# Optimization experiments

Measured on AMD Instinct MI355X. Metric: run time of the kernel, lower is better.

The kernel has to match this reference:

```python
import jax, jax.numpy as jnp
import numpy as np

SEQ, BATCH, HIDDEN = 2048, 1, 4096
NUM_HEADS, NUM_KV_HEADS, HEAD_DIM = 32, 8, 128
Q_PER_GROUP = NUM_HEADS // NUM_KV_HEADS  # 4
TOTAL_PROJ = NUM_KV_HEADS * (Q_PER_GROUP + 2) * HEAD_DIM  # 6144


def setup_inputs() -> dict:
    key = jax.random.key(0)
    k1, k2, k3 = jax.random.split(key, 3)
    tokens = jax.random.normal(k1, (SEQ, BATCH, HIDDEN), dtype=jnp.float32)
    # xavier-ish scaling so activations stay sane
    weight_qkv = jax.random.normal(k2, (TOTAL_PROJ, HIDDEN), dtype=jnp.float32) * (2.0 / (TOTAL_PROJ + HIDDEN)) ** 0.5
    weight_proj = jax.random.normal(k3, (HIDDEN, NUM_HEADS * HEAD_DIM), dtype=jnp.float32) * (2.0 / (HIDDEN + NUM_HEADS * HEAD_DIM)) ** 0.5
    return {"tokens": tokens, "weight_qkv": weight_qkv, "weight_proj": weight_proj}


def reference(tokens, weight_qkv, weight_proj):
    S, B, H = tokens.shape
    scale = 1.0 / HEAD_DIM ** 0.5
    # QKV projection with interleaved GQA layout: per KV group [q0..q_{g-1}, k, v]
    qkv = jnp.einsum('sbh,ph->sbp', tokens, weight_qkv)
    qkv = qkv.reshape(S, B, NUM_KV_HEADS, Q_PER_GROUP + 2, HEAD_DIM)
    q = qkv[:, :, :, :Q_PER_GROUP, :].reshape(S, B, NUM_HEADS, HEAD_DIM)
    k = qkv[:, :, :, Q_PER_GROUP, :]       # [S,B,KVH,D]
    v = qkv[:, :, :, Q_PER_GROUP + 1, :]
    # repeat_interleave KV heads to match Q heads (GQA)
    k = jnp.repeat(k, Q_PER_GROUP, axis=2)
    v = jnp.repeat(v, Q_PER_GROUP, axis=2)
    # [S,B,H,D] -> [B,H,S,D]
    q = q.transpose(1, 2, 0, 3)
    k = k.transpose(1, 2, 0, 3)
    v = v.transpose(1, 2, 0, 3)
    scores = jnp.einsum('bhsd,bhtd->bhst', q, k) * scale
    causal = jnp.tril(jnp.ones((S, S), dtype=bool))
    scores = jnp.where(causal, scores, jnp.finfo(scores.dtype).min)
    attn = jax.nn.softmax(scores, axis=-1)
    out = jnp.einsum('bhst,bhtd->bhsd', attn, v)
    # [B,H,S,D] -> [S,B,H*D]
    out = out.transpose(2, 0, 1, 3).reshape(S, B, NUM_HEADS * HEAD_DIM)
    return jnp.einsum('sbe,he->sbh', out, weight_proj)
```

## Files before the change

### kernel.cpp

```cpp
#include <hip/hip_runtime.h>
#include <hip/hip_bf16.h>
#include <stdint.h>

#define SEQ 2048
#define HIDDEN 4096
#define NHEADS 32
#define HD 128
#define QKV_LD 6144
#define OUT_LD 4096

typedef __attribute__((ext_vector_type(8))) short short8;
typedef __attribute__((ext_vector_type(4))) short short4v;
typedef __attribute__((ext_vector_type(4))) float f32x4;
typedef __attribute__((ext_vector_type(4))) int int4v;
typedef __attribute__((ext_vector_type(2))) unsigned int uint2v;
typedef __attribute__((ext_vector_type(4))) float float4v;

__device__ __forceinline__ short f2bf(float f) {
  uint32_t u = __builtin_bit_cast(uint32_t, f);
  u += 0x7fff + ((u >> 16) & 1);
  return (short)(u >> 16);
}

__global__ void cast_kernel(const float* __restrict__ in, short* __restrict__ out, int n4) {
  int stride = gridDim.x * blockDim.x;
  for (int i = blockIdx.x * blockDim.x + threadIdx.x; i < n4; i += stride) {
    float4v v = ((const float4v*)in)[i];
    short4v o;
    o[0] = f2bf(v[0]); o[1] = f2bf(v[1]); o[2] = f2bf(v[2]); o[3] = f2bf(v[3]);
    ((short4v*)out)[i] = o;
  }
}

template <typename OT, int NBF>
__global__ __launch_bounds__(512, 2) void gemm256b(const short* __restrict__ A,
                                                   const short* __restrict__ B,
                                                   OT* __restrict__ C,
                                                   int M, int N, int K, int NT) {
  __shared__ __align__(16) short lds[32768 + NBF * 8192];
  const int tid = threadIdx.x;
  const int w = tid >> 6, lane = tid & 63;
  const int wr = w >> 2, wc = w & 3;
  const int llo = lane & 15, lhi = lane >> 4;

  const int nwg = gridDim.x;
  const int cpx = nwg >> 3;
  const int work = ((int)blockIdx.x & 7) * cpx + ((int)blockIdx.x >> 3);
  const int mt = work / NT, nt = work % NT;
  const size_t arow0 = (size_t)mt * 256, brow0 = (size_t)nt * (NBF * 64);
  const short* Ab = A + arow0 * K;
  const short* Bb = B + brow0 * K;

  f32x4 acc[8][NBF] = {};

  auto STAGE_A = [&](int kt, int j) {
    const int bufd = kt & 1;
    const int r0 = (j << 6) + (w << 3);
    const int row = r0 + (lane >> 3);
    const short* src = Ab + (size_t)row * K + (kt << 6) + (((lane & 7) ^ (row & 7)) << 3);
    short* dst = lds + (bufd << 14) + r0 * 64;
    __builtin_amdgcn_global_load_lds(
        (const __attribute__((address_space(1))) uint32_t*)src,
        (__attribute__((address_space(3))) uint32_t*)dst, 16, 0, 0);
  };
  auto STAGE_B = [&](int kt, int j) {
    const int bufd = kt & 1;
    const int r0 = (j << 6) + (w << 3);
    const int row = r0 + (lane >> 3);
    const short* src = Bb + (size_t)row * K + (kt << 6) + (((lane & 7) ^ (row & 7)) << 3);
    short* dst = lds + 32768 + bufd * (NBF << 12) + r0 * 64;
    __builtin_amdgcn_global_load_lds(
        (const __attribute__((address_space(1))) uint32_t*)src,
        (__attribute__((address_space(3))) uint32_t*)dst, 16, 0, 0);
  };
  auto STAGE = [&](int kt) {
#pragma unroll
    for (int j = 0; j < 4; j++) STAGE_A(kt, j);
#pragma unroll
    for (int j = 0; j < NBF; j++) STAGE_B(kt, j);
  };

  auto LDA = [&](int bufd, int m, int kk) -> short8 {
    const int row = (wr << 7) + (m << 4) + llo;
    const int ch = ((kk << 2) + lhi) ^ (row & 7);
    return *(const short8*)(lds + (bufd << 14) + row * 64 + (ch << 3));
  };
  auto LDB = [&](int bufd, int n, int kk) -> short8 {
    const int row = wc * (NBF << 4) + (n << 4) + llo;
    const int ch = ((kk << 2) + lhi) ^ (row & 7);
    return *(const short8*)(lds + 32768 + bufd * (NBF << 12) + row * 64 + (ch << 3));
  };

  STAGE(0);
  STAGE(1);
  if constexpr (NBF == 3) asm volatile("s_waitcnt vmcnt(7)" ::: "memory");
  else                    asm volatile("s_waitcnt vmcnt(6)" ::: "memory");
  __builtin_amdgcn_s_barrier();

  const int NKT = K >> 6;
  for (int kt = 0; kt < NKT; ++kt) {
    const int bufd = kt & 1;
    short8 b_[NBF][2];
#pragma unroll
    for (int n = 0; n < NBF; n++) { b_[n][0] = LDB(bufd, n, 0); b_[n][1] = LDB(bufd, n, 1); }
#pragma unroll
    for (int m = 0; m < 8; m++) {
      short8 a0 = LDA(bufd, m, 0);
      short8 a1 = LDA(bufd, m, 1);
#pragma unroll
      for (int n = 0; n < NBF; n++) {
        acc[m][n] = __builtin_amdgcn_mfma_f32_16x16x32_bf16(a0, b_[n][0], acc[m][n], 0, 0, 0);
        acc[m][n] = __builtin_amdgcn_mfma_f32_16x16x32_bf16(a1, b_[n][1], acc[m][n], 0, 0, 0);
      }
    }
    asm volatile("s_waitcnt lgkmcnt(0)" ::: "memory");
    __builtin_amdgcn_s_barrier();
    if (kt + 2 < NKT) STAGE(kt + 2);
    if (kt + 1 < NKT) {
      if (kt + 2 < NKT) {
        if constexpr (NBF == 3) asm volatile("s_waitcnt vmcnt(7)" ::: "memory");
        else                    asm volatile("s_waitcnt vmcnt(6)" ::: "memory");
      } else {
        asm volatile("s_waitcnt vmcnt(0)" ::: "memory");
      }
      __builtin_amdgcn_s_barrier();
    }
  }

#pragma unroll
  for (int m = 0; m < 8; m++)
#pragma unroll
    for (int n = 0; n < NBF; n++)
#pragma unroll
      for (int r = 0; r < 4; r++) {
        const size_t row = arow0 + (wr << 7) + (m << 4) + (lhi << 2) + r;
        const size_t col = brow0 + wc * (NBF << 4) + (n << 4) + llo;
        const float v = acc[m][n][r];
        if constexpr (sizeof(OT) == 2) C[row * N + col] = f2bf(v);
        else                           C[row * N + col] = v;
      }
}

__global__ __launch_bounds__(512) void attn_fwd(const short* __restrict__ qkv,
                                                short* __restrict__ aout) {
  const int qt = gridDim.y - 1 - blockIdx.y;
  const int h = blockIdx.x;
  const int kvh = h >> 2, g = h & 3;
  const int tid = threadIdx.x;
  const int wave = tid >> 6, lane = tid & 63;
  const int lhi = lane >> 4, llo = lane & 15;

  __shared__ __align__(16) short Ksm[2][64 * 128];
  __shared__ __align__(16) short Vsm[2][64 * 128];
  __shared__ __align__(16) short Psm[8][16 * 72];

  const float scale = 0.08838834764831845f;

  const int qrow = qt * 128 + wave * 16 + llo;
  const short* qbase = qkv + (size_t)qrow * QKV_LD + (kvh * 6 + g) * HD;
  short8 qf[4];
#pragma unroll
  for (int kk = 0; kk < 4; kk++) qf[kk] = *(const short8*)(qbase + kk * 32 + lhi * 8);

  f32x4 o[8] = {};
  float mrow[4], lrow[4];
#pragma unroll
  for (int r = 0; r < 4; r++) { mrow[r] = -1e30f; lrow[r] = 0.f; }

  const short* Kg = qkv + (kvh * 6 + 4) * HD;
  const short* Vg = qkv + (kvh * 6 + 5) * HD;

  auto STAGE_K = [&](int t, int buf) {
#pragma unroll
    for (int c = 0; c < 2; c++) {
      const int call = wave * 2 + c;
      const int row = call * 4 + lhi;
      const int sc = llo ^ (row & 7);
      __builtin_amdgcn_global_load_lds(
          (const __attribute__((address_space(1))) uint32_t*)(Kg + (size_t)(t * 64 + row) * QKV_LD + sc * 8),
          (__attribute__((address_space(3))) uint32_t*)(&Ksm[buf][0] + call * 512), 16, 0, 0);
    }
  };
  short8 vreg[2];
  auto LOAD_V = [&](int t) {
#pragma unroll
    for (int c = 0; c < 2; c++) {
      const int idx = c * 512 + tid;
      const int vr = idx >> 4;
      vreg[c] = *(const short8*)(Vg + (size_t)(t * 64 + vr) * QKV_LD + (idx & 15) * 8);
    }
  };
  auto WRITE_V = [&](int buf) {
#pragma unroll
    for (int c = 0; c < 2; c++) {
      const int idx = c * 512 + tid;
      const int vr = idx >> 4, vc = idx & 15;
      *(short8*)(&Vsm[buf][0] + ((vr >> 2) * 8 + (vc >> 1)) * 64 + (vr & 3) * 16 + (vc & 1) * 8) = vreg[c];
    }
  };

  const uint32_t vlane0 = (uint32_t)(uintptr_t)(__attribute__((address_space(3))) short*)(&Vsm[0][0])
                          + (uint32_t)(lhi * 2048 + llo * 8);

  STAGE_K(0, 0);
  LOAD_V(0);
  asm volatile("s_waitcnt vmcnt(0)" ::: "memory");
  WRITE_V(0);
  __syncthreads();

  const int ntiles = 2 * qt + 2;
  const int qpos0 = qt * 128 + wave * 16 + lhi * 4;
  for (int t = 0; t < ntiles; t++) {
    const int cur = t & 1, nxt = cur ^ 1;
    const bool pf = (t + 1 < ntiles);
    if (pf) { STAGE_K(t + 1, nxt); LOAD_V(t + 1); }

    const short* Kc = &Ksm[cur][0];
    f32x4 s[4] = {};
#pragma unroll
    for (int n = 0; n < 4; n++) {
#pragma unroll
      for (int kk = 0; kk < 4; kk++) {
        const int krow = n * 16 + llo;
        const int ch = (kk * 4 + lhi) ^ (krow & 7);
        short8 kf = *(const short8*)(Kc + krow * 128 + ch * 8);
        s[n] = __builtin_amdgcn_mfma_f32_16x16x32_bf16(qf[kk], kf, s[n], 0, 0, 0);
      }
    }

    float sv[4][4];
    const bool diag = (t >= 2 * qt);
#pragma unroll
    for (int n = 0; n < 4; n++)
#pragma unroll
      for (int r = 0; r < 4; r++) {
        float x = s[n][r] * scale;
        if (diag && (t * 64 + n * 16 + llo > qpos0 + r)) x = -1e30f;
        sv[n][r] = x;
      }

    float rm4[4];
#pragma unroll
    for (int r = 0; r < 4; r++) {
      float rm = fmaxf(fmaxf(sv[0][r], sv[1][r]), fmaxf(sv[2][r], sv[3][r]));
#pragma unroll
      for (int msk = 1; msk < 16; msk <<= 1) rm = fmaxf(rm, __shfl_xor(rm, msk));
      rm4[r] = rm;
    }
    bool need = false;
#pragma unroll
    for (int r = 0; r < 4; r++) need = need || (rm4[r] > mrow[r] + 8.0f);
    if (__any(need)) {
#pragma unroll
      for (int r = 0; r < 4; r++) {
        const float mnew = fmaxf(mrow[r], rm4[r]);
        const float a = __expf(mrow[r] - mnew);
        mrow[r] = mnew;
        lrow[r] *= a;
#pragma unroll
        for (int nn = 0; nn < 8; nn++) o[nn][r] *= a;
      }
    }
#pragma unroll
    for (int r = 0; r < 4; r++) {
      float rs = 0.f;
#pragma unroll
      for (int n = 0; n < 4; n++) {
        float p = __expf(sv[n][r] - mrow[r]);
        sv[n][r] = p;
        rs += p;
      }
#pragma unroll
      for (int msk = 1; msk < 16; msk <<= 1) rs += __shfl_xor(rs, msk);
      lrow[r] += rs;
    }

    short* P = &Psm[wave][0];
#pragma unroll
    for (int n = 0; n < 4; n++)
#pragma unroll
      for (int r = 0; r < 4; r++)
        P[(lhi * 4 + r) * 72 + n * 16 + llo] = f2bf(sv[n][r]);

    short8 pa0 = *(const short8*)(P + llo * 72 + lhi * 8);
    short8 pa1 = *(const short8*)(P + llo * 72 + 32 + lhi * 8);
    const uint32_t vlane = vlane0 + (uint32_t)(cur * 16384);
#pragma unroll
    for (int ks = 0; ks < 2; ks++) {
      uint2v vr_[8][2];
#pragma unroll
      for (int nn = 0; nn < 8; nn++)
#pragma unroll
        for (int hh = 0; hh < 2; hh++) {
          uint32_t a = vlane + (uint32_t)(ks * 8192 + hh * 1024 + nn * 128);
          asm volatile("ds_read_b64_tr_b16 %0, %1" : "=v"(vr_[nn][hh]) : "v"(a));
        }
      asm volatile("s_waitcnt lgkmcnt(0)" ::: "memory");
      __builtin_amdgcn_sched_barrier(0);
      const short8 pa = ks ? pa1 : pa0;
#pragma unroll
      for (int nn = 0; nn < 8; nn++) {
        int4v tv;
        tv[0] = (int)vr_[nn][0][0]; tv[1] = (int)vr_[nn][0][1];
        tv[2] = (int)vr_[nn][1][0]; tv[3] = (int)vr_[nn][1][1];
        o[nn] = __builtin_amdgcn_mfma_f32_16x16x32_bf16(pa, __builtin_bit_cast(short8, tv), o[nn], 0, 0, 0);
      }
    }

    if (pf) {
      asm volatile("s_waitcnt vmcnt(0)" ::: "memory");
      __syncthreads();
      WRITE_V(nxt);
      __syncthreads();
    }
  }

#pragma unroll
  for (int nn = 0; nn < 8; nn++)
#pragma unroll
    for (int r = 0; r < 4; r++) {
      const size_t row = qt * 128 + wave * 16 + lhi * 4 + r;
      const size_t col = (size_t)h * HD + nn * 16 + llo;
      aout[row * OUT_LD + col] = f2bf(o[nn][r] / lrow[r]);
    }
}

extern "C" void kernel_launch(void* const* d_in, const int* in_sizes, int n_in,
                              void* d_out, int out_size, void* d_ws, size_t ws_size,
                              hipStream_t stream) {
  const float* tokens = (const float*)d_in[0];
  const float* wqkv   = (const float*)d_in[1];
  const float* wproj  = (const float*)d_in[2];
  float* out = (float*)d_out;

  short* tok_bf   = (short*)d_ws;
  short* wqkv_bf  = tok_bf   + (size_t)SEQ * HIDDEN;
  short* wproj_bf = wqkv_bf  + (size_t)QKV_LD * HIDDEN;
  short* qkv_bf   = wproj_bf + (size_t)HIDDEN * OUT_LD;
  short* attn_bf  = qkv_bf   + (size_t)SEQ * QKV_LD;

  cast_kernel<<<2048, 256, 0, stream>>>(tokens, tok_bf, SEQ * HIDDEN / 4);
  cast_kernel<<<2048, 256, 0, stream>>>(wqkv, wqkv_bf, QKV_LD * HIDDEN / 4);
  cast_kernel<<<2048, 256, 0, stream>>>(wproj, wproj_bf, HIDDEN * OUT_LD / 4);

  gemm256b<short, 3><<<256, 512, 0, stream>>>(tok_bf, wqkv_bf, qkv_bf, SEQ, QKV_LD, HIDDEN, QKV_LD / 192);

  attn_fwd<<<dim3(NHEADS, SEQ / 128), 512, 0, stream>>>(qkv_bf, attn_bf);

  gemm256b<float, 2><<<256, 512, 0, stream>>>(attn_bf, wproj_bf, out, SEQ, OUT_LD, HIDDEN, OUT_LD / 128);
}
```

Before: 319.0 us.

## Remap GEMM tile order per XCD and streamline attention softmax with exp2

The GEMM work-index mapping now assigns each XCD a contiguous range of N tiles, with M tiles as the fast index, so blocks on the same XCD share B panels in L2. In attention, log2(e) is folded into the softmax scale and exp2f replaces __expf, saving a multiply per exponential. The causal mask is split into separate diagonal and non-diagonal branches so off-diagonal tiles skip the compare. V transpose reads now use the immediate offset field instead of per-read address adds. The new GEMM mapping assumes exactly 8 M tiles (mt = i & 7), so it is only correct for grids of that shape.

Result: no change. 316.7 us (-0.7%).

```diff
diff --git a/kernel.cpp b/kernel.cpp
--- a/kernel.cpp
+++ b/kernel.cpp
@@ -43,10 +43,10 @@
   const int wr = w >> 2, wc = w & 3;
   const int llo = lane & 15, lhi = lane >> 4;
 
-  const int nwg = gridDim.x;
-  const int cpx = nwg >> 3;
-  const int work = ((int)blockIdx.x & 7) * cpx + ((int)blockIdx.x >> 3);
-  const int mt = work / NT, nt = work % NT;
+  const int xcd = (int)blockIdx.x & 7;
+  const int i = (int)blockIdx.x >> 3;
+  const int nt = xcd * (NT >> 3) + (i >> 3);
+  const int mt = i & 7;
   const size_t arow0 = (size_t)mt * 256, brow0 = (size_t)nt * (NBF * 64);
   const short* Ab = A + arow0 * K;
   const short* Bb = B + brow0 * K;
@@ -154,7 +154,7 @@
   __shared__ __align__(16) short Vsm[2][64 * 128];
   __shared__ __align__(16) short Psm[8][16 * 72];
 
-  const float scale = 0.08838834764831845f;
+  const float scale2 = 0.08838834764831845f * 1.4426950408889634f;
 
   const int qrow = qt * 128 + wave * 16 + llo;
   const short* qbase = qkv + (size_t)qrow * QKV_LD + (kvh * 6 + g) * HD;
@@ -229,15 +229,21 @@
     }
 
     float sv[4][4];
-    const bool diag = (t >= 2 * qt);
-#pragma unroll
-    for (int n = 0; n < 4; n++)
-#pragma unroll
-      for (int r = 0; r < 4; r++) {
-        float x = s[n][r] * scale;
-        if (diag && (t * 64 + n * 16 + llo > qpos0 + r)) x = -1e30f;
-        sv[n][r] = x;
-      }
+    if (t >= 2 * qt) {
+#pragma unroll
+      for (int n = 0; n < 4; n++)
+#pragma unroll
+        for (int r = 0; r < 4; r++) {
+          float x = s[n][r] * scale2;
+          if (t * 64 + n * 16 + llo > qpos0 + r) x = -1e30f;
+          sv[n][r] = x;
+        }
+    } else {
+#pragma unroll
+      for (int n = 0; n < 4; n++)
+#pragma unroll
+        for (int r = 0; r < 4; r++) sv[n][r] = s[n][r] * scale2;
+    }
 
     float rm4[4];
 #pragma unroll
@@ -254,7 +260,7 @@
 #pragma unroll
       for (int r = 0; r < 4; r++) {
         const float mnew = fmaxf(mrow[r], rm4[r]);
-        const float a = __expf(mrow[r] - mnew);
+        const float a = exp2f(mrow[r] - mnew);
         mrow[r] = mnew;
         lrow[r] *= a;
 #pragma unroll
@@ -266,7 +272,7 @@
       float rs = 0.f;
 #pragma unroll
       for (int n = 0; n < 4; n++) {
-        float p = __expf(sv[n][r] - mrow[r]);
+        float p = exp2f(sv[n][r] - mrow[r]);
         sv[n][r] = p;
         rs += p;
       }
@@ -284,7 +290,7 @@
 
     short8 pa0 = *(const short8*)(P + llo * 72 + lhi * 8);
     short8 pa1 = *(const short8*)(P + llo * 72 + 32 + lhi * 8);
-    const uint32_t vlane = vlane0 + (uint32_t)(cur * 16384);
+    const uint32_t vbase = vlane0 + (uint32_t)(cur * 16384);
 #pragma unroll
     for (int ks = 0; ks < 2; ks++) {
       uint2v vr_[8][2];
@@ -292,8 +298,9 @@
       for (int nn = 0; nn < 8; nn++)
 #pragma unroll
         for (int hh = 0; hh < 2; hh++) {
-          uint32_t a = vlane + (uint32_t)(ks * 8192 + hh * 1024 + nn * 128);
-          asm volatile("ds_read_b64_tr_b16 %0, %1" : "=v"(vr_[nn][hh]) : "v"(a));
+          asm volatile("ds_read_b64_tr_b16 %0, %1 offset:%2"
+                       : "=v"(vr_[nn][hh])
+                       : "v"(vbase), "i"(ks * 8192 + hh * 1024 + nn * 128));
         }
       asm volatile("s_waitcnt lgkmcnt(0)" ::: "memory");
       __builtin_amdgcn_sched_barrier(0);
```
